# Kernel optimization log

Measured on AMD Instinct MI355X. Metric: run time of the kernel, lower is better.

Reference implementation:

```python
import jax, jax.numpy as jnp
import numpy as np

TEMPERATURE = 0.2
EPS = 1e-8  # torch F.cosine_similarity eps


def setup_inputs() -> dict:
    key = jax.random.key(0)
    k1, k2, k3 = jax.random.split(key, 3)
    N, D, K = 2048, 512, 65536
    query = jax.random.normal(k1, (N, D), dtype=jnp.float32)
    keys = jax.random.normal(k2, (N, D), dtype=jnp.float32)
    queue = jax.random.normal(k3, (K, D), dtype=jnp.float32)
    return {"query": query, "keys": keys, "queue": queue}


def reference(query, keys, queue):
    # Norms
    qn = jnp.linalg.norm(query, axis=-1)   # [N]
    kn = jnp.linalg.norm(keys, axis=-1)    # [N]
    un = jnp.linalg.norm(queue, axis=-1)   # [K]
    # Positive logits: only the diagonal of the NxN cosine-sim is used,
    # so compute row-wise dot products directly.  [N]
    l_pos = jnp.sum(query * keys, axis=-1) / jnp.maximum(qn * kn, EPS) / TEMPERATURE
    # Negative logits via GEMM then normalize.  [N, K]
    l_neg = jnp.einsum('nd,kd->nk', query, queue)
    l_neg = l_neg / jnp.maximum(qn[:, None] * un[None, :], EPS) / TEMPERATURE
    # logits = [l_pos | l_neg], labels are all 0 -> CE = mean(logsumexp - logit_0)
    logits = jnp.concatenate([l_pos[:, None], l_neg], axis=1)  # [N, K+1]
    lse = jax.nn.logsumexp(logits, axis=1)                     # [N]
    loss = jnp.mean(lse - l_pos)
    return loss
```

## Files before the change

kernel.cpp:

```cpp
#include <hip/hip_runtime.h>
#include <hip/hip_bf16.h>
#include <math.h>

#define N_ROWS 2048
#define D_DIM  512
#define K_NEG  65536
#define INV_T  5.0f
#define NC     4
#define NT     (NC * 16)

typedef __bf16 bf16x8 __attribute__((ext_vector_type(8)));
typedef float  f32x4  __attribute__((ext_vector_type(4)));

__device__ __forceinline__ void gload_lds16(const __bf16* g, __bf16* l) {
    __builtin_amdgcn_global_load_lds(
        (const __attribute__((address_space(1))) void*)g,
        (__attribute__((address_space(3))) void*)l, 16, 0, 0);
}

__global__ __launch_bounds__(256) void prep_all_kernel(
    const float* __restrict__ query, const float* __restrict__ keys,
    const float* __restrict__ queue,
    __bf16* __restrict__ Abf, __bf16* __restrict__ Bbf,
    float* __restrict__ sq, float* __restrict__ ru,
    float* __restrict__ lpos, float* __restrict__ rowsum) {
    const int lane = threadIdx.x & 63;
    if (blockIdx.x < N_ROWS / 4) {
        const int row = blockIdx.x * 4 + (threadIdx.x >> 6);
        const float4* qv = reinterpret_cast<const float4*>(query + (size_t)row * D_DIM) + lane * 2;
        const float4* kv = reinterpret_cast<const float4*>(keys  + (size_t)row * D_DIM) + lane * 2;
        float4 q0 = qv[0], q1 = qv[1];
        float4 k0 = kv[0], k1 = kv[1];
        float ssq = q0.x*q0.x + q0.y*q0.y + q0.z*q0.z + q0.w*q0.w
                  + q1.x*q1.x + q1.y*q1.y + q1.z*q1.z + q1.w*q1.w;
        float ssk = k0.x*k0.x + k0.y*k0.y + k0.z*k0.z + k0.w*k0.w
                  + k1.x*k1.x + k1.y*k1.y + k1.z*k1.z + k1.w*k1.w;
        float dot = q0.x*k0.x + q0.y*k0.y + q0.z*k0.z + q0.w*k0.w
                  + q1.x*k1.x + q1.y*k1.y + q1.z*k1.z + q1.w*k1.w;
#pragma unroll
        for (int off = 32; off > 0; off >>= 1) {
            ssq += __shfl_xor(ssq, off, 64);
            ssk += __shfl_xor(ssk, off, 64);
            dot += __shfl_xor(dot, off, 64);
        }
        bf16x8 o;
        o[0] = (__bf16)q0.x; o[1] = (__bf16)q0.y; o[2] = (__bf16)q0.z; o[3] = (__bf16)q0.w;
        o[4] = (__bf16)q1.x; o[5] = (__bf16)q1.y; o[6] = (__bf16)q1.z; o[7] = (__bf16)q1.w;
        reinterpret_cast<bf16x8*>(Abf + (size_t)row * D_DIM)[lane] = o;
        if (lane == 0) {
            float qn = sqrtf(ssq), kn = sqrtf(ssk);
            float lp = dot / fmaxf(qn * kn, 1e-8f) * INV_T;
            sq[row]     = INV_T / fmaxf(qn, 1e-8f);
            lpos[row]   = lp;
            rowsum[row] = __expf(lp);
        }
    } else {
        const int row = (blockIdx.x - N_ROWS / 4) * 4 + (threadIdx.x >> 6);
        const float4* uv = reinterpret_cast<const float4*>(queue + (size_t)row * D_DIM) + lane * 2;
        float4 u0 = uv[0], u1 = uv[1];
        float ss = u0.x*u0.x + u0.y*u0.y + u0.z*u0.z + u0.w*u0.w
                 + u1.x*u1.x + u1.y*u1.y + u1.z*u1.z + u1.w*u1.w;
#pragma unroll
        for (int off = 32; off > 0; off >>= 1) ss += __shfl_xor(ss, off, 64);
        bf16x8 o;
        o[0] = (__bf16)u0.x; o[1] = (__bf16)u0.y; o[2] = (__bf16)u0.z; o[3] = (__bf16)u0.w;
        o[4] = (__bf16)u1.x; o[5] = (__bf16)u1.y; o[6] = (__bf16)u1.z; o[7] = (__bf16)u1.w;
        reinterpret_cast<bf16x8*>(Bbf + (size_t)row * D_DIM)[lane] = o;
        if (lane == 0) ru[row] = 1.0f / fmaxf(sqrtf(ss), 1e-8f);
    }
}

__global__ __launch_bounds__(256, 3) void gemm_exp_kernel(
    const __bf16* __restrict__ A, const __bf16* __restrict__ B,
    const float* __restrict__ sq, const float* __restrict__ ru,
    float* __restrict__ rowsum) {
    __shared__ __bf16 sA[2 * 4096];
    __shared__ __bf16 sB[2 * 4096];
    const int tid  = threadIdx.x;
    const int wave = tid >> 6, lane = tid & 63;
    const int rowBlock = blockIdx.x;
    const int colGroup = blockIdx.y;

    const int wm = wave >> 1, wn = wave & 1;
    const int q4 = lane >> 4, m16 = lane & 15;

    const int r4 = lane >> 2, c2 = lane & 3;
    const int gsw = c2 ^ ((r4 >> 1) & 3);
    const int j0 = wave, j1 = wave + 4;
    const __bf16* gA  = A + (((size_t)(rowBlock * 128 + r4)) << 9) + (gsw << 3);
    const __bf16* gB0 = B + (((size_t)(colGroup * NC * 128 + r4)) << 9) + (gsw << 3);
    const int rsw = (q4 ^ ((m16 >> 1) & 3)) << 3;

    float sqv[4][4];
#pragma unroll
    for (int i = 0; i < 4; ++i)
#pragma unroll
        for (int r = 0; r < 4; ++r)
            sqv[i][r] = sq[rowBlock * 128 + wm * 64 + i * 16 + q4 * 4 + r];

    float srow[4][4] = {{0.f,0.f,0.f,0.f},{0.f,0.f,0.f,0.f},
                        {0.f,0.f,0.f,0.f},{0.f,0.f,0.f,0.f}};
    f32x4 acc[4][4] = {};

#define STAGE(T, BUF) do {                                                        \
        const int cb_ = (T) >> 4, kof_ = ((T) & 15) * 32;                         \
        const __bf16* gBc_ = gB0 + ((size_t)cb_ << 16);                           \
        __bf16* dA_ = &sA[(BUF) * 4096];                                          \
        __bf16* dB_ = &sB[(BUF) * 4096];                                          \
        gload_lds16(gA  + (size_t)j0 * 16 * D_DIM + kof_, &dA_[j0 * 512]);        \
        gload_lds16(gA  + (size_t)j1 * 16 * D_DIM + kof_, &dA_[j1 * 512]);        \
        gload_lds16(gBc_ + (size_t)j0 * 16 * D_DIM + kof_, &dB_[j0 * 512]);       \
        gload_lds16(gBc_ + (size_t)j1 * 16 * D_DIM + kof_, &dB_[j1 * 512]);       \
    } while (0)

    STAGE(0, 0);

    for (int t = 0; t < NT; ++t) {
        const int cur = t & 1;
        __syncthreads();
        if (t + 1 < NT) STAGE(t + 1, cur ^ 1);

        const __bf16* bA = &sA[cur * 4096];
        const __bf16* bB = &sB[cur * 4096];
        bf16x8 af[4], bq[4];
#pragma unroll
        for (int i = 0; i < 4; ++i)
            af[i] = *reinterpret_cast<const bf16x8*>(&bA[(wm * 64 + i * 16 + m16) * 32 + rsw]);
#pragma unroll
        for (int j = 0; j < 4; ++j)
            bq[j] = *reinterpret_cast<const bf16x8*>(&bB[(wn * 64 + j * 16 + m16) * 32 + rsw]);
#pragma unroll
        for (int i = 0; i < 4; ++i)
#pragma unroll
            for (int j = 0; j < 4; ++j)
                acc[i][j] = __builtin_amdgcn_mfma_f32_16x16x32_bf16(af[i], bq[j], acc[i][j], 0, 0, 0);

        if ((t & 15) == 15) {
            const int colBlock = colGroup * NC + (t >> 4);
            float ruv[4];
#pragma unroll
            for (int j = 0; j < 4; ++j)
                ruv[j] = ru[colBlock * 128 + wn * 64 + j * 16 + m16];
#pragma unroll
            for (int i = 0; i < 4; ++i)
#pragma unroll
                for (int r = 0; r < 4; ++r) {
                    float s = 0.f;
#pragma unroll
                    for (int j = 0; j < 4; ++j)
                        s += __expf(acc[i][j][r] * sqv[i][r] * ruv[j]);
                    srow[i][r] += s;
                    acc[i][0][r] = 0.f; acc[i][1][r] = 0.f;
                    acc[i][2][r] = 0.f; acc[i][3][r] = 0.f;
                }
        }
    }
#undef STAGE

#pragma unroll
    for (int i = 0; i < 4; ++i)
#pragma unroll
        for (int r = 0; r < 4; ++r) {
            float s = srow[i][r];
#pragma unroll
            for (int off = 1; off < 16; off <<= 1)
                s += __shfl_xor(s, off, 64);
            if (m16 == 0) {
                const int grow = rowBlock * 128 + wm * 64 + i * 16 + q4 * 4 + r;
                atomicAdd(&rowsum[grow], s);
            }
        }
}

__global__ __launch_bounds__(256) void finalize_kernel(
    const float* __restrict__ rowsum, const float* __restrict__ lpos,
    float* __restrict__ out) {
    const int tid = threadIdx.x;
    float acc = 0.f;
    for (int n = tid; n < N_ROWS; n += 256)
        acc += __logf(rowsum[n]) - lpos[n];
#pragma unroll
    for (int off = 32; off > 0; off >>= 1) acc += __shfl_xor(acc, off, 64);
    __shared__ float red[4];
    if ((tid & 63) == 0) red[tid >> 6] = acc;
    __syncthreads();
    if (tid == 0) out[0] = (red[0] + red[1] + red[2] + red[3]) * (1.0f / (float)N_ROWS);
}

extern "C" void kernel_launch(void* const* d_in, const int* in_sizes, int n_in,
                              void* d_out, int out_size, void* d_ws, size_t ws_size,
                              hipStream_t stream) {
    const float* query = (const float*)d_in[0];
    const float* keys  = (const float*)d_in[1];
    const float* queue = (const float*)d_in[2];

    char* ws = (char*)d_ws;
    __bf16* Abf = (__bf16*)ws;  ws += (size_t)N_ROWS * D_DIM * sizeof(__bf16);
    __bf16* Bbf = (__bf16*)ws;  ws += (size_t)K_NEG  * D_DIM * sizeof(__bf16);
    float*  sq   = (float*)ws;  ws += (size_t)N_ROWS * sizeof(float);
    float*  ru   = (float*)ws;  ws += (size_t)K_NEG  * sizeof(float);
    float*  lpos = (float*)ws;  ws += (size_t)N_ROWS * sizeof(float);
    float*  rsum = (float*)ws;  ws += (size_t)N_ROWS * sizeof(float);

    prep_all_kernel<<<N_ROWS / 4 + K_NEG / 4, 256, 0, stream>>>(
        query, keys, queue, Abf, Bbf, sq, ru, lpos, rsum);
    gemm_exp_kernel<<<dim3(N_ROWS / 128, K_NEG / 128 / NC), 256, 0, stream>>>(
        Abf, Bbf, sq, ru, rsum);
    finalize_kernel<<<1, 256, 0, stream>>>(rsum, lpos, (float*)d_out);
}
```

Before: 383.8 us.

## Fold norm scaling into bf16 operands and triple-buffer GEMM loads with vmcnt waits

The prep kernel now multiplies query rows by INV_T/||q|| and queue rows by 1/||u|| before the bf16 cast. This removes the sq/ru arrays and the per-element scale multiplies in the GEMM epilogue. The GEMM main loop moves from double to triple buffering in LDS with prefetch distance two, using explicit s_waitcnt vmcnt plus s_barrier instead of __syncthreads, and the chunk loop is restructured so the exp epilogue sits outside the k-loop. Pre-scaling before rounding to bf16 slightly changes numerics, and the extra buffer raises LDS use to 48KB per block, which may limit occupancy.

```diff
diff --git a/kernel.cpp b/kernel.cpp
--- a/kernel.cpp
+++ b/kernel.cpp
@@ -22,7 +22,6 @@
     const float* __restrict__ query, const float* __restrict__ keys,
     const float* __restrict__ queue,
     __bf16* __restrict__ Abf, __bf16* __restrict__ Bbf,
-    float* __restrict__ sq, float* __restrict__ ru,
     float* __restrict__ lpos, float* __restrict__ rowsum) {
     const int lane = threadIdx.x & 63;
     if (blockIdx.x < N_ROWS / 4) {
@@ -43,14 +42,16 @@
             ssk += __shfl_xor(ssk, off, 64);
             dot += __shfl_xor(dot, off, 64);
         }
+        const float qn = sqrtf(ssq), kn = sqrtf(ssk);
+        const float aS = INV_T / fmaxf(qn, 1e-8f);
         bf16x8 o;
-        o[0] = (__bf16)q0.x; o[1] = (__bf16)q0.y; o[2] = (__bf16)q0.z; o[3] = (__bf16)q0.w;
-        o[4] = (__bf16)q1.x; o[5] = (__bf16)q1.y; o[6] = (__bf16)q1.z; o[7] = (__bf16)q1.w;
+        o[0] = (__bf16)(q0.x*aS); o[1] = (__bf16)(q0.y*aS);
+        o[2] = (__bf16)(q0.z*aS); o[3] = (__bf16)(q0.w*aS);
+        o[4] = (__bf16)(q1.x*aS); o[5] = (__bf16)(q1.y*aS);
+        o[6] = (__bf16)(q1.z*aS); o[7] = (__bf16)(q1.w*aS);
         reinterpret_cast<bf16x8*>(Abf + (size_t)row * D_DIM)[lane] = o;
         if (lane == 0) {
-            float qn = sqrtf(ssq), kn = sqrtf(ssk);
             float lp = dot / fmaxf(qn * kn, 1e-8f) * INV_T;
-            sq[row]     = INV_T / fmaxf(qn, 1e-8f);
             lpos[row]   = lp;
             rowsum[row] = __expf(lp);
         }
@@ -62,20 +63,20 @@
                  + u1.x*u1.x + u1.y*u1.y + u1.z*u1.z + u1.w*u1.w;
 #pragma unroll
         for (int off = 32; off > 0; off >>= 1) ss += __shfl_xor(ss, off, 64);
+        const float uS = 1.0f / fmaxf(sqrtf(ss), 1e-8f);
         bf16x8 o;
-        o[0] = (__bf16)u0.x; o[1] = (__bf16)u0.y; o[2] = (__bf16)u0.z; o[3] = (__bf16)u0.w;
-        o[4] = (__bf16)u1.x; o[5] = (__bf16)u1.y; o[6] = (__bf16)u1.z; o[7] = (__bf16)u1.w;
+        o[0] = (__bf16)(u0.x*uS); o[1] = (__bf16)(u0.y*uS);
+        o[2] = (__bf16)(u0.z*uS); o[3] = (__bf16)(u0.w*uS);
+        o[4] = (__bf16)(u1.x*uS); o[5] = (__bf16)(u1.y*uS);
+        o[6] = (__bf16)(u1.z*uS); o[7] = (__bf16)(u1.w*uS);
         reinterpret_cast<bf16x8*>(Bbf + (size_t)row * D_DIM)[lane] = o;
-        if (lane == 0) ru[row] = 1.0f / fmaxf(sqrtf(ss), 1e-8f);
     }
 }
 
 __global__ __launch_bounds__(256, 3) void gemm_exp_kernel(
     const __bf16* __restrict__ A, const __bf16* __restrict__ B,
-    const float* __restrict__ sq, const float* __restrict__ ru,
     float* __restrict__ rowsum) {
-    __shared__ __bf16 sA[2 * 4096];
-    __shared__ __bf16 sB[2 * 4096];
+    __shared__ __bf16 sAB[3][2][4096];
     const int tid  = threadIdx.x;
     const int wave = tid >> 6, lane = tid & 63;
     const int rowBlock = blockIdx.x;
@@ -91,13 +92,6 @@
     const __bf16* gB0 = B + (((size_t)(colGroup * NC * 128 + r4)) << 9) + (gsw << 3);
     const int rsw = (q4 ^ ((m16 >> 1) & 3)) << 3;
 
-    float sqv[4][4];
-#pragma unroll
-    for (int i = 0; i < 4; ++i)
-#pragma unroll
-        for (int r = 0; r < 4; ++r)
-            sqv[i][r] = sq[rowBlock * 128 + wm * 64 + i * 16 + q4 * 4 + r];
-
     float srow[4][4] = {{0.f,0.f,0.f,0.f},{0.f,0.f,0.f,0.f},
                         {0.f,0.f,0.f,0.f},{0.f,0.f,0.f,0.f}};
     f32x4 acc[4][4] = {};
@@ -105,8 +99,8 @@
 #define STAGE(T, BUF) do {                                                        \
         const int cb_ = (T) >> 4, kof_ = ((T) & 15) * 32;                         \
         const __bf16* gBc_ = gB0 + ((size_t)cb_ << 16);                           \
-        __bf16* dA_ = &sA[(BUF) * 4096];                                          \
-        __bf16* dB_ = &sB[(BUF) * 4096];                                          \
+        __bf16* dA_ = &sAB[(BUF)][0][0];                                          \
+        __bf16* dB_ = &sAB[(BUF)][1][0];                                          \
         gload_lds16(gA  + (size_t)j0 * 16 * D_DIM + kof_, &dA_[j0 * 512]);        \
         gload_lds16(gA  + (size_t)j1 * 16 * D_DIM + kof_, &dA_[j1 * 512]);        \
         gload_lds16(gBc_ + (size_t)j0 * 16 * D_DIM + kof_, &dB_[j0 * 512]);       \
@@ -114,46 +108,52 @@
     } while (0)
 
     STAGE(0, 0);
-
-    for (int t = 0; t < NT; ++t) {
-        const int cur = t & 1;
-        __syncthreads();
-        if (t + 1 < NT) STAGE(t + 1, cur ^ 1);
-
-        const __bf16* bA = &sA[cur * 4096];
-        const __bf16* bB = &sB[cur * 4096];
-        bf16x8 af[4], bq[4];
+    STAGE(1, 1);
+
+    int bufR = 0, bufW = 2;
+#pragma unroll
+    for (int c = 0; c < NC; ++c) {
+        for (int kt = 0; kt < 16; ++kt) {
+            const int t = c * 16 + kt;
+            if (t + 1 < NT)
+                asm volatile("s_waitcnt vmcnt(4)\n\ts_barrier" ::: "memory");
+            else
+                asm volatile("s_waitcnt vmcnt(0)\n\ts_barrier" ::: "memory");
+            if (t + 2 < NT) STAGE(t + 2, bufW);
+
+            const __bf16* bA = &sAB[bufR][0][0];
+            const __bf16* bB = &sAB[bufR][1][0];
+            bf16x8 af[4], bq[4];
+#pragma unroll
+            for (int i = 0; i < 4; ++i)
+                af[i] = *reinterpret_cast<const bf16x8*>(&bA[(wm * 64 + i * 16 + m16) * 32 + rsw]);
+#pragma unroll
+            for (int j = 0; j < 4; ++j)
+                bq[j] = *reinterpret_cast<const bf16x8*>(&bB[(wn * 64 + j * 16 + m16) * 32 + rsw]);
+#pragma unroll
+            for (int i = 0; i < 4; ++i)
+#pragma unroll
+                for (int j = 0; j < 4; ++j)
+                    acc[i][j] = __builtin_amdgcn_mfma_f32_16x16x32_bf16(af[i], bq[j], acc[i][j], 0, 0, 0);
+
+            bufR = (bufR == 2) ? 0 : bufR + 1;
+            bufW = (bufW == 2) ? 0 : bufW + 1;
+        }
 #pragma unroll
         for (int i = 0; i < 4; ++i)
-            af[i] = *reinterpret_cast<const bf16x8*>(&bA[(wm * 64 + i * 16 + m16) * 32 + rsw]);
-#pragma unroll
-        for (int j = 0; j < 4; ++j)
-            bq[j] = *reinterpret_cast<const bf16x8*>(&bB[(wn * 64 + j * 16 + m16) * 32 + rsw]);
+#pragma unroll
+            for (int r = 0; r < 4; ++r) {
+                float s = 0.f;
+#pragma unroll
+                for (int j = 0; j < 4; ++j)
+                    s += __expf(acc[i][j][r]);
+                srow[i][r] += s;
+            }
 #pragma unroll
         for (int i = 0; i < 4; ++i)
 #pragma unroll
             for (int j = 0; j < 4; ++j)
-                acc[i][j] = __builtin_amdgcn_mfma_f32_16x16x32_bf16(af[i], bq[j], acc[i][j], 0, 0, 0);
-
-        if ((t & 15) == 15) {
-            const int colBlock = colGroup * NC + (t >> 4);
-            float ruv[4];
-#pragma unroll
-            for (int j = 0; j < 4; ++j)
-                ruv[j] = ru[colBlock * 128 + wn * 64 + j * 16 + m16];
-#pragma unroll
-            for (int i = 0; i < 4; ++i)
-#pragma unroll
-                for (int r = 0; r < 4; ++r) {
-                    float s = 0.f;
-#pragma unroll
-                    for (int j = 0; j < 4; ++j)
-                        s += __expf(acc[i][j][r] * sqv[i][r] * ruv[j]);
-                    srow[i][r] += s;
-                    acc[i][0][r] = 0.f; acc[i][1][r] = 0.f;
-                    acc[i][2][r] = 0.f; acc[i][3][r] = 0.f;
-                }
-        }
+                acc[i][j] = f32x4{0.f, 0.f, 0.f, 0.f};
     }
 #undef STAGE
 
@@ -197,14 +197,12 @@
     char* ws = (char*)d_ws;
     __bf16* Abf = (__bf16*)ws;  ws += (size_t)N_ROWS * D_DIM * sizeof(__bf16);
     __bf16* Bbf = (__bf16*)ws;  ws += (size_t)K_NEG  * D_DIM * sizeof(__bf16);
-    float*  sq   = (float*)ws;  ws += (size_t)N_ROWS * sizeof(float);
-    float*  ru   = (float*)ws;  ws += (size_t)K_NEG  * sizeof(float);
     float*  lpos = (float*)ws;  ws += (size_t)N_ROWS * sizeof(float);
     float*  rsum = (float*)ws;  ws += (size_t)N_ROWS * sizeof(float);
 
     prep_all_kernel<<<N_ROWS / 4 + K_NEG / 4, 256, 0, stream>>>(
-        query, keys, queue, Abf, Bbf, sq, ru, lpos, rsum);
+        query, keys, queue, Abf, Bbf, lpos, rsum);
     gemm_exp_kernel<<<dim3(N_ROWS / 128, K_NEG / 128 / NC), 256, 0, stream>>>(
-        Abf, Bbf, sq, ru, rsum);
+        Abf, Bbf, rsum);
     finalize_kernel<<<1, 256, 0, stream>>>(rsum, lpos, (float*)d_out);
 }
```

Result: slower. 533.8 us (+39.1%).
